# Performance work log

Measured on AMD Instinct MI355X. Metric: run time of the kernel, lower is better.

The kernel has to match this reference:

```python
import jax, jax.numpy as jnp
import numpy as np

D_MODEL = 1024
D_STATE = 16
D_CONV = 4
D_INNER = 2048  # expand * d_model
BATCH = 2
LENGTH = 2048


def silu(u):
    return u * jax.nn.sigmoid(u)


def setup_inputs() -> dict:
    key = jax.random.key(0)
    ks = jax.random.split(key, 8)
    sc = 0.02
    x = jax.random.normal(ks[0], (BATCH, LENGTH, D_MODEL), jnp.float32)
    W_in = jax.random.normal(ks[1], (2 * D_INNER, D_MODEL), jnp.float32) * sc
    conv_w = jax.random.normal(ks[2], (D_INNER, 1, D_CONV), jnp.float32) * 0.1
    conv_b = jnp.zeros((D_INNER,), jnp.float32)
    W_x = jax.random.normal(ks[3], (D_INNER + 2 * D_STATE, D_INNER), jnp.float32) * sc
    W_dt = jax.random.normal(ks[4], (D_INNER, D_INNER), jnp.float32) * sc
    b_dt = jnp.zeros((D_INNER,), jnp.float32)
    # A = arange(1, d_state+1) repeated for each inner channel (per source init)
    A_log = jnp.log(jnp.tile(jnp.arange(1, D_STATE + 1, dtype=jnp.float32), (D_INNER, 1)))
    D = jnp.ones((D_INNER,), jnp.float32)
    W_out = jax.random.normal(ks[5], (D_MODEL, D_INNER), jnp.float32) * sc
    ln_g = jnp.ones((D_MODEL,), jnp.float32)
    ln_b = jnp.zeros((D_MODEL,), jnp.float32)
    return dict(x=x, W_in=W_in, conv_w=conv_w, conv_b=conv_b, W_x=W_x, W_dt=W_dt,
                b_dt=b_dt, A_log=A_log, D=D, W_out=W_out, ln_g=ln_g, ln_b=ln_b)


def reference(x, W_in, conv_w, conv_b, W_x, W_dt, b_dt, A_log, D, W_out, ln_g, ln_b):
    b, l, _ = x.shape
    residual = x
    # in_proj, split into x-path and gate z
    xz = x @ W_in.T  # (b, l, 2*d_inner)
    xs, z = jnp.split(xz, 2, axis=-1)
    # depthwise causal conv1d (left pad d_conv-1, take first l outputs)
    xc = jnp.transpose(xs, (0, 2, 1))  # (b, d_inner, l)
    xc = jax.lax.conv_general_dilated(
        xc, conv_w, window_strides=(1,), padding=[(D_CONV - 1, 0)],
        dimension_numbers=('NCH', 'OIH', 'NCH'), feature_group_count=D_INNER)
    xc = xc + conv_b[None, :, None]
    u = silu(jnp.transpose(xc, (0, 2, 1)))  # (b, l, d_inner)
    # SSM parameter projection
    proj = u @ W_x.T  # (b, l, d_inner + 2*d_state)
    d_in, Bm, Cm = jnp.split(proj, [D_INNER, D_INNER + D_STATE], axis=-1)
    delta = jax.nn.softplus(d_in @ W_dt.T + b_dt)  # (b, l, d_inner)
    A = -jnp.exp(A_log)  # (d_inner, d_state)
    dA = jnp.exp(delta[..., None] * A)                         # (b, l, d, n)
    dBu = delta[..., None] * Bm[:, :, None, :] * u[..., None]  # (b, l, d, n)

    def step(state, inp):
        dA_t, dBu_t, c_t = inp
        state = state * dA_t + dBu_t            # (b, d, n)
        y_t = jnp.einsum('bdn,bn->bd', state, c_t)
        return state, y_t

    init = jnp.zeros((b, D_INNER, D_STATE), x.dtype)
    _, ys = jax.lax.scan(step, init, (jnp.transpose(dA, (1, 0, 2, 3)),
                                      jnp.transpose(dBu, (1, 0, 2, 3)),
                                      jnp.transpose(Cm, (1, 0, 2))))
    y = jnp.transpose(ys, (1, 0, 2)) + u * D  # (b, l, d_inner)
    y = y * silu(z)
    out = y @ W_out.T + residual
    mu = jnp.mean(out, axis=-1, keepdims=True)
    var = jnp.var(out, axis=-1, keepdims=True)
    return (out - mu) / jnp.sqrt(var + 1e-5) * ln_g + ln_b
```

## Files before the change

### kernel.cpp

```cpp
#include <hip/hip_runtime.h>

typedef unsigned short u16;
typedef unsigned int u32;
typedef __bf16 bf16x8_t __attribute__((ext_vector_type(8)));
typedef float f32x4_t __attribute__((ext_vector_type(4)));


#define NCH 64
#define CLEN 32

__device__ __forceinline__ u16 f2bf(float f) {
  u32 u = __float_as_uint(f);
  return (u16)((u + 0x7fffu + ((u >> 16) & 1u)) >> 16);
}
__device__ __forceinline__ float bf2f(u16 h) { return __uint_as_float(((u32)h) << 16); }

__device__ __forceinline__ void async_ld16(const u16* g, u16* l) {
  __builtin_amdgcn_global_load_lds((const __attribute__((address_space(1))) void*)g,
                                   (__attribute__((address_space(3))) void*)l, 16, 0, 0);
}

__global__ void k_cvt_all(const float* __restrict__ x, u16* __restrict__ x_bf,
                          const float* __restrict__ W_in, u16* __restrict__ Win_bf,
                          const float* __restrict__ W_x, u16* __restrict__ Wx_bf,
                          const float* __restrict__ W_dt, u16* __restrict__ Wdt_bf,
                          const float* __restrict__ W_out, u16* __restrict__ Wout_bf) {
  int g = blockIdx.x * 256 + threadIdx.x;
  const float* src;
  u16* dst;
  int rel;
  bool valid = true;
  if (g < 1048576) { src = x; dst = x_bf; rel = g; }
  else if (g < 2097152) { src = W_in; dst = Win_bf; rel = g - 1048576; }
  else if (g < 3211264) { src = W_x; dst = Wx_bf; rel = g - 2097152; valid = rel < 1064960; }
  else if (g < 4259840) { src = W_dt; dst = Wdt_bf; rel = g - 3211264; }
  else if (g < 4784128) { src = W_out; dst = Wout_bf; rel = g - 4259840; }
  else return;
  u32 lo = 0, hi = 0;
  if (valid) {
    float4 v = reinterpret_cast<const float4*>(src)[rel];
    lo = (u32)f2bf(v.x) | ((u32)f2bf(v.y) << 16);
    hi = (u32)f2bf(v.z) | ((u32)f2bf(v.w) << 16);
  }
  reinterpret_cast<uint2*>(dst)[rel] = make_uint2(lo, hi);
}

__global__ void k_transpose(const u16* __restrict__ in, u16* __restrict__ out) {
  __shared__ u16 tile[64][72];
  int bx = blockIdx.x;
  int by = blockIdx.y;
  int t = threadIdx.x;
#pragma unroll
  for (int i = 0; i < 2; ++i) {
    int idx = i * 256 + t;
    int r = idx >> 3;
    int c = (idx & 7) * 8;
    *reinterpret_cast<uint4*>(&tile[r][c]) =
        *reinterpret_cast<const uint4*>(in + (size_t)(by * 64 + r) * 2048 + bx * 64 + c);
  }
  __syncthreads();
#pragma unroll
  for (int i = 0; i < 2; ++i) {
    int idx = i * 256 + t;
    int r = idx >> 3;
    int c = (idx & 7) * 8;
    u16 tmp[8];
#pragma unroll
    for (int e = 0; e < 8; ++e) tmp[e] = tile[c + e][r];
    *reinterpret_cast<uint4*>(out + (size_t)(bx * 64 + r) * 2048 + by * 64 + c) =
        *reinterpret_cast<uint4*>(tmp);
  }
}

template <bool WB, bool WF>
__global__ __launch_bounds__(256, 2) void k_gemm_bt(
    const u16* __restrict__ A, int lda, const u16* __restrict__ B, int ldb,
    float* __restrict__ Cf, int ldcf, size_t fsplit,
    u16* __restrict__ Cb, int ldc, int K) {
  __shared__ __align__(16) u16 sA[128 * 64];
  __shared__ __align__(16) u16 sB[128 * 64];
  const int tid = threadIdx.x;
  const int lane = tid & 63;
  const int wave = tid >> 6;
  const size_t tm = (size_t)blockIdx.y * 128;
  const size_t tn = (size_t)blockIdx.x * 128;
  const int kbase = blockIdx.z * K;
  const int wm = (wave & 1) * 64;
  const int wn = (wave >> 1) * 64;
  const int mrow = lane & 15;
  const int quad = lane >> 4;

  f32x4_t acc[4][4];
#pragma unroll
  for (int i = 0; i < 4; ++i)
#pragma unroll
    for (int j = 0; j < 4; ++j) {
      acc[i][j][0] = 0.f; acc[i][j][1] = 0.f; acc[i][j][2] = 0.f; acc[i][j][3] = 0.f;
    }

  for (int k0 = 0; k0 < K; k0 += 64) {
#pragma unroll
    for (int j = 0; j < 4; ++j) {
      int idx = j * 256 + tid;
      int row = idx >> 3;
      int col = (idx & 7) << 3;
      async_ld16(A + (tm + row) * (size_t)lda + (kbase + k0 + col), sA + (size_t)idx * 8);
      async_ld16(B + (tn + row) * (size_t)ldb + (kbase + k0 + col), sB + (size_t)idx * 8);
    }
    __syncthreads();
#pragma unroll
    for (int kk = 0; kk < 64; kk += 32) {
      bf16x8_t af[4], bfr[4];
#pragma unroll
      for (int i = 0; i < 4; ++i)
        af[i] = *reinterpret_cast<const bf16x8_t*>(sA + (wm + i * 16 + mrow) * 64 + kk + quad * 8);
#pragma unroll
      for (int i = 0; i < 4; ++i)
        bfr[i] = *reinterpret_cast<const bf16x8_t*>(sB + (wn + i * 16 + mrow) * 64 + kk + quad * 8);
#pragma unroll
      for (int i = 0; i < 4; ++i)
#pragma unroll
        for (int j = 0; j < 4; ++j)
          acc[i][j] = __builtin_amdgcn_mfma_f32_16x16x32_bf16(af[i], bfr[j], acc[i][j], 0, 0, 0);
    }
    __syncthreads();
  }

  if (WF) Cf += (size_t)blockIdx.z * fsplit;
#pragma unroll
  for (int i = 0; i < 4; ++i)
#pragma unroll
    for (int j = 0; j < 4; ++j) {
      size_t r0 = tm + wm + i * 16 + quad * 4;
      size_t c = tn + wn + j * 16 + mrow;
#pragma unroll
      for (int r = 0; r < 4; ++r) {
        float v = acc[i][j][r];
        if (WF) Cf[(r0 + r) * (size_t)ldcf + c] = v;
        if (WB) Cb[(r0 + r) * (size_t)ldc + c] = f2bf(v);
      }
    }
}

__global__ void k_bc_reduce(const float* __restrict__ part, float* __restrict__ projBC) {
  int g = blockIdx.x * 256 + threadIdx.x;
  int r = g >> 3, c4 = (g & 7) * 4;
  size_t idx = (size_t)r * 128 + c4;
  float4 a = *reinterpret_cast<const float4*>(part + idx);
  float4 b = *reinterpret_cast<const float4*>(part + 524288 + idx);
  float4 c = *reinterpret_cast<const float4*>(part + 1048576 + idx);
  float4 d = *reinterpret_cast<const float4*>(part + 1572864 + idx);
  float4 o;
  o.x = a.x + b.x + c.x + d.x;
  o.y = a.y + b.y + c.y + d.y;
  o.z = a.z + b.z + c.z + d.z;
  o.w = a.w + b.w + c.w + d.w;
  *reinterpret_cast<float4*>(projBC + idx) = o;
}

__global__ void k_conv_silu(const u16* __restrict__ xz, const float* __restrict__ cw,
                            const float* __restrict__ cb, u16* __restrict__ u) {
  int bl = blockIdx.x;
  int l = bl & 2047;
  int d0 = threadIdx.x * 8;
  float acc[8];
  float4 cb0 = *reinterpret_cast<const float4*>(cb + d0);
  float4 cb1 = *reinterpret_cast<const float4*>(cb + d0 + 4);
  acc[0] = cb0.x; acc[1] = cb0.y; acc[2] = cb0.z; acc[3] = cb0.w;
  acc[4] = cb1.x; acc[5] = cb1.y; acc[6] = cb1.z; acc[7] = cb1.w;
  float4 w[8];
#pragma unroll
  for (int i = 0; i < 8; ++i) w[i] = *reinterpret_cast<const float4*>(cw + (d0 + i) * 4);
#pragma unroll
  for (int k = 0; k < 4; ++k) {
    int lp = l + k - 3;
    if (lp >= 0) {
      bf16x8_t xv = *reinterpret_cast<const bf16x8_t*>(xz + ((size_t)(bl + k - 3) << 12) + d0);
#pragma unroll
      for (int i = 0; i < 8; ++i)
        acc[i] += (float)xv[i] * reinterpret_cast<const float*>(&w[i])[k];
    }
  }
  u16 tmp[8];
#pragma unroll
  for (int i = 0; i < 8; ++i) {
    float s = acc[i] / (1.f + __expf(-acc[i]));
    tmp[i] = f2bf(s);
  }
  *reinterpret_cast<uint4*>(u + ((size_t)bl << 11) + d0) = *reinterpret_cast<uint4*>(tmp);
}

__device__ __forceinline__ float softplus_fast(float x) {
  return __logf(1.f + __expf(x));
}

__global__ void k_scan1(const u16* __restrict__ dpre, const float* __restrict__ bdt,
                        const u16* __restrict__ u, const float* __restrict__ projBC,
                        const float* __restrict__ A_log, float* __restrict__ sF,
                        float* __restrict__ aF) {
  int d = blockIdx.x * 256 + threadIdx.x;
  int c = blockIdx.y, b = blockIdx.z;
  float A[16], s[16], ap[16];
#pragma unroll
  for (int q = 0; q < 4; ++q) {
    float4 al = reinterpret_cast<const float4*>(A_log + d * 16)[q];
    A[q * 4 + 0] = -__expf(al.x); A[q * 4 + 1] = -__expf(al.y);
    A[q * 4 + 2] = -__expf(al.z); A[q * 4 + 3] = -__expf(al.w);
  }
#pragma unroll
  for (int n = 0; n < 16; ++n) { s[n] = 0.f; ap[n] = 1.f; }
  float bd = bdt[d];
  int t0 = c * CLEN;
  for (int t = t0; t < t0 + CLEN; ++t) {
    size_t rb = (size_t)(b * 2048 + t);
    float delta = softplus_fast(bf2f(dpre[rb * 2048 + d]) + bd);
    float du = delta * bf2f(u[rb * 2048 + d]);
    const float4* Bp = reinterpret_cast<const float4*>(projBC + rb * 128);
    float4 B0 = Bp[0], B1 = Bp[1], B2 = Bp[2], B3 = Bp[3];
    float Bv[16] = {B0.x, B0.y, B0.z, B0.w, B1.x, B1.y, B1.z, B1.w,
                    B2.x, B2.y, B2.z, B2.w, B3.x, B3.y, B3.z, B3.w};
#pragma unroll
    for (int n = 0; n < 16; ++n) {
      float dA = __expf(delta * A[n]);
      s[n] = fmaf(s[n], dA, du * Bv[n]);
      ap[n] *= dA;
    }
  }
  size_t o = ((size_t)((b * NCH + c) * 2048 + d)) << 4;
#pragma unroll
  for (int q = 0; q < 4; ++q) {
    reinterpret_cast<float4*>(sF + o)[q] = make_float4(s[q * 4], s[q * 4 + 1], s[q * 4 + 2], s[q * 4 + 3]);
    reinterpret_cast<float4*>(aF + o)[q] = make_float4(ap[q * 4], ap[q * 4 + 1], ap[q * 4 + 2], ap[q * 4 + 3]);
  }
}

__global__ void k_scan_carry(const float* __restrict__ sF, const float* __restrict__ aF,
                             float* __restrict__ carry) {
  int g = blockIdx.x * 256 + threadIdx.x;
  int b = g >> 15;
  int dn = g & 32767;
  float S = 0.f;
#pragma unroll 4
  for (int c = 0; c < NCH; ++c) {
    size_t idx = ((size_t)(b * NCH + c) << 15) + dn;
    carry[idx] = S;
    S = S * aF[idx] + sF[idx];
  }
}

__global__ void k_scan3(const u16* __restrict__ dpre, const float* __restrict__ bdt,
                        const u16* __restrict__ u, const float* __restrict__ projBC,
                        const float* __restrict__ A_log, const float* __restrict__ carry,
                        const float* __restrict__ Dvec, const u16* __restrict__ xz,
                        u16* __restrict__ ybf) {
  int d = blockIdx.x * 256 + threadIdx.x;
  int c = blockIdx.y, b = blockIdx.z;
  float A[16], s[16];
#pragma unroll
  for (int q = 0; q < 4; ++q) {
    float4 al = reinterpret_cast<const float4*>(A_log + d * 16)[q];
    A[q * 4 + 0] = -__expf(al.x); A[q * 4 + 1] = -__expf(al.y);
    A[q * 4 + 2] = -__expf(al.z); A[q * 4 + 3] = -__expf(al.w);
  }
  size_t o = ((size_t)((b * NCH + c) * 2048 + d)) << 4;
#pragma unroll
  for (int q = 0; q < 4; ++q) {
    float4 cv = reinterpret_cast<const float4*>(carry + o)[q];
    s[q * 4] = cv.x; s[q * 4 + 1] = cv.y; s[q * 4 + 2] = cv.z; s[q * 4 + 3] = cv.w;
  }
  float bd = bdt[d];
  float Dd = Dvec[d];
  int t0 = c * CLEN;
  for (int t = t0; t < t0 + CLEN; ++t) {
    size_t rb = (size_t)(b * 2048 + t);
    float delta = softplus_fast(bf2f(dpre[rb * 2048 + d]) + bd);
    float uv = bf2f(u[rb * 2048 + d]);
    float du = delta * uv;
    const float4* Bp = reinterpret_cast<const float4*>(projBC + rb * 128);
    float4 B0 = Bp[0], B1 = Bp[1], B2 = Bp[2], B3 = Bp[3];
    float4 C0 = Bp[4], C1 = Bp[5], C2 = Bp[6], C3 = Bp[7];
    float Bv[16] = {B0.x, B0.y, B0.z, B0.w, B1.x, B1.y, B1.z, B1.w,
                    B2.x, B2.y, B2.z, B2.w, B3.x, B3.y, B3.z, B3.w};
    float Cv[16] = {C0.x, C0.y, C0.z, C0.w, C1.x, C1.y, C1.z, C1.w,
                    C2.x, C2.y, C2.z, C2.w, C3.x, C3.y, C3.z, C3.w};
    float yv = 0.f;
#pragma unroll
    for (int n = 0; n < 16; ++n) {
      float dA = __expf(delta * A[n]);
      s[n] = fmaf(s[n], dA, du * Bv[n]);
      yv = fmaf(s[n], Cv[n], yv);
    }
    yv += uv * Dd;
    float z = bf2f(xz[(rb << 12) + 2048 + d]);
    yv *= z / (1.f + __expf(-z));
    ybf[rb * 2048 + d] = f2bf(yv);
  }
}

__global__ void k_ln(const float* __restrict__ pre, const float* __restrict__ x,
                     const float* __restrict__ gam, const float* __restrict__ bet,
                     float* __restrict__ out) {
  int row = blockIdx.x, tid = threadIdx.x;
  size_t base = (size_t)row * 1024 + tid * 4;
  float4 v = *reinterpret_cast<const float4*>(pre + base);
  float4 p1 = *reinterpret_cast<const float4*>(pre + 4194304 + base);
  float4 r = *reinterpret_cast<const float4*>(x + base);
  v.x += p1.x + r.x; v.y += p1.y + r.y; v.z += p1.z + r.z; v.w += p1.w + r.w;
  float s = v.x + v.y + v.z + v.w;
  float s2 = v.x * v.x + v.y * v.y + v.z * v.z + v.w * v.w;
#pragma unroll
  for (int o = 32; o >= 1; o >>= 1) {
    s += __shfl_xor(s, o);
    s2 += __shfl_xor(s2, o);
  }
  __shared__ float red[8];
  int lane = tid & 63, wv = tid >> 6;
  if (lane == 0) { red[wv] = s; red[4 + wv] = s2; }
  __syncthreads();
  s = red[0] + red[1] + red[2] + red[3];
  s2 = red[4] + red[5] + red[6] + red[7];
  float mu = s * (1.f / 1024.f);
  float var = s2 * (1.f / 1024.f) - mu * mu;
  float rstd = rsqrtf(var + 1e-5f);
  float4 gg = *reinterpret_cast<const float4*>(gam + tid * 4);
  float4 bb = *reinterpret_cast<const float4*>(bet + tid * 4);
  float4 o;
  o.x = (v.x - mu) * rstd * gg.x + bb.x;
  o.y = (v.y - mu) * rstd * gg.y + bb.y;
  o.z = (v.z - mu) * rstd * gg.z + bb.z;
  o.w = (v.w - mu) * rstd * gg.w + bb.w;
  *reinterpret_cast<float4*>(out + base) = o;
}

extern "C" void kernel_launch(void* const* d_in, const int* in_sizes, int n_in,
                              void* d_out, int out_size, void* d_ws, size_t ws_size,
                              hipStream_t stream) {
  (void)in_sizes; (void)n_in; (void)out_size; (void)ws_size;
  const float* x = (const float*)d_in[0];
  const float* W_in = (const float*)d_in[1];
  const float* conv_w = (const float*)d_in[2];
  const float* conv_b = (const float*)d_in[3];
  const float* W_x = (const float*)d_in[4];
  const float* W_dt = (const float*)d_in[5];
  const float* b_dt = (const float*)d_in[6];
  const float* A_log = (const float*)d_in[7];
  const float* Dv = (const float*)d_in[8];
  const float* W_out = (const float*)d_in[9];
  const float* ln_g = (const float*)d_in[10];
  const float* ln_b = (const float*)d_in[11];
  float* out = (float*)d_out;

  char* p = (char*)d_ws;
  u16* xz_bf = (u16*)p;      p += (size_t)4096 * 4096 * 2;
  u16* u_bf = (u16*)p;       p += (size_t)4096 * 2048 * 2;
  float* projBC = (float*)p; p += (size_t)4096 * 128 * 4;
  u16* dpre_bf = (u16*)p;    p += (size_t)4096 * 2048 * 2;
  u16* ybf = (u16*)p;        p += (size_t)4096 * 2048 * 2;
  float* sF = (float*)p;     p += (size_t)2 * NCH * 2048 * 16 * 4;
  float* aF = (float*)p;     p += (size_t)2 * NCH * 2048 * 16 * 4;
  float* carry = (float*)p;  p += (size_t)2 * NCH * 2048 * 16 * 4;
  u16* Wx_bf = (u16*)p;      p += (size_t)2176 * 2048 * 2;
  u16* WxT_bf = (u16*)p;     p += (size_t)2048 * 2048 * 2;
  u16* Weff_bf = (u16*)p;    p += (size_t)2048 * 2048 * 2;
  u16* Wdt_bf = (u16*)p;     p += (size_t)2048 * 2048 * 2;
  u16* Wout_bf = (u16*)p;    p += (size_t)1024 * 2048 * 2;
  u16* x_bf = (u16*)p;       p += (size_t)4096 * 1024 * 2;
  u16* Win_bf = (u16*)p;     p += (size_t)4096 * 1024 * 2;
  float* BCpart = sF;
  float* outpre = sF;

  k_cvt_all<<<18688, 256, 0, stream>>>(x, x_bf, W_in, Win_bf, W_x, Wx_bf, W_dt, Wdt_bf,
                                       W_out, Wout_bf);
  k_transpose<<<dim3(32, 32), 256, 0, stream>>>(Wx_bf, WxT_bf);
  k_gemm_bt<true, false><<<dim3(16, 16), 256, 0, stream>>>(
      Wdt_bf, 2048, WxT_bf, 2048, nullptr, 0, 0, Weff_bf, 2048, 2048);
  k_gemm_bt<true, false><<<dim3(32, 32), 256, 0, stream>>>(
      x_bf, 1024, Win_bf, 1024, nullptr, 0, 0, xz_bf, 4096, 1024);
  k_conv_silu<<<4096, 256, 0, stream>>>(xz_bf, conv_w, conv_b, u_bf);
  k_gemm_bt<false, true><<<dim3(1, 32, 4), 256, 0, stream>>>(
      u_bf, 2048, Wx_bf + (size_t)2048 * 2048, 2048, BCpart, 128, (size_t)4096 * 128,
      nullptr, 0, 512);
  k_bc_reduce<<<128, 256, 0, stream>>>(BCpart, projBC);
  k_gemm_bt<true, false><<<dim3(16, 32), 256, 0, stream>>>(
      u_bf, 2048, Weff_bf, 2048, nullptr, 0, 0, dpre_bf, 2048, 2048);
  k_scan1<<<dim3(8, NCH, 2), 256, 0, stream>>>(dpre_bf, b_dt, u_bf, projBC, A_log, sF, aF);
  k_scan_carry<<<256, 256, 0, stream>>>(sF, aF, carry);
  k_scan3<<<dim3(8, NCH, 2), 256, 0, stream>>>(dpre_bf, b_dt, u_bf, projBC, A_log, carry,
                                               Dv, xz_bf, ybf);
  k_gemm_bt<false, true><<<dim3(8, 32, 2), 256, 0, stream>>>(
      ybf, 2048, Wout_bf, 2048, outpre, 1024, (size_t)4096 * 1024, nullptr, 0, 1024);
  k_ln<<<4096, 256, 0, stream>>>(outpre, x, ln_g, ln_b, out);
}
```

Measured before the change: 453.3 us.

## Merge prep kernels, co-launch independent GEMMs, fold B/C projection into delta GEMM

```diff
diff --git a/kernel.cpp b/kernel.cpp
--- a/kernel.cpp
+++ b/kernel.cpp
@@ -20,71 +20,73 @@
                                    (__attribute__((address_space(3))) void*)l, 16, 0, 0);
 }
 
-__global__ void k_cvt_all(const float* __restrict__ x, u16* __restrict__ x_bf,
-                          const float* __restrict__ W_in, u16* __restrict__ Win_bf,
-                          const float* __restrict__ W_x, u16* __restrict__ Wx_bf,
-                          const float* __restrict__ W_dt, u16* __restrict__ Wdt_bf,
-                          const float* __restrict__ W_out, u16* __restrict__ Wout_bf) {
-  int g = blockIdx.x * 256 + threadIdx.x;
-  const float* src;
-  u16* dst;
-  int rel;
-  bool valid = true;
-  if (g < 1048576) { src = x; dst = x_bf; rel = g; }
-  else if (g < 2097152) { src = W_in; dst = Win_bf; rel = g - 1048576; }
-  else if (g < 3211264) { src = W_x; dst = Wx_bf; rel = g - 2097152; valid = rel < 1064960; }
-  else if (g < 4259840) { src = W_dt; dst = Wdt_bf; rel = g - 3211264; }
-  else if (g < 4784128) { src = W_out; dst = Wout_bf; rel = g - 4259840; }
-  else return;
-  u32 lo = 0, hi = 0;
-  if (valid) {
-    float4 v = reinterpret_cast<const float4*>(src)[rel];
-    lo = (u32)f2bf(v.x) | ((u32)f2bf(v.y) << 16);
-    hi = (u32)f2bf(v.z) | ((u32)f2bf(v.w) << 16);
-  }
-  reinterpret_cast<uint2*>(dst)[rel] = make_uint2(lo, hi);
-}
-
-__global__ void k_transpose(const u16* __restrict__ in, u16* __restrict__ out) {
+__global__ void k_prep(const float* __restrict__ x, u16* __restrict__ x_bf,
+                       const float* __restrict__ W_in, u16* __restrict__ Win_bf,
+                       const float* __restrict__ W_dt, u16* __restrict__ Wdt_bf,
+                       const float* __restrict__ W_out, u16* __restrict__ Wout_bf,
+                       const float* __restrict__ W_x, u16* __restrict__ WxT,
+                       u16* __restrict__ Weff_ext) {
   __shared__ u16 tile[64][72];
-  int bx = blockIdx.x;
-  int by = blockIdx.y;
-  int t = threadIdx.x;
-#pragma unroll
-  for (int i = 0; i < 2; ++i) {
-    int idx = i * 256 + t;
-    int r = idx >> 3;
-    int c = (idx & 7) * 8;
-    *reinterpret_cast<uint4*>(&tile[r][c]) =
-        *reinterpret_cast<const uint4*>(in + (size_t)(by * 64 + r) * 2048 + bx * 64 + c);
-  }
-  __syncthreads();
-#pragma unroll
-  for (int i = 0; i < 2; ++i) {
-    int idx = i * 256 + t;
-    int r = idx >> 3;
-    int c = (idx & 7) * 8;
-    u16 tmp[8];
-#pragma unroll
-    for (int e = 0; e < 8; ++e) tmp[e] = tile[c + e][r];
-    *reinterpret_cast<uint4*>(out + (size_t)(bx * 64 + r) * 2048 + by * 64 + c) =
-        *reinterpret_cast<uint4*>(tmp);
+  int blk = blockIdx.x;
+  if (blk < 14592) {
+    int g = blk * 256 + threadIdx.x;
+    const float* src;
+    u16* dst;
+    int rel;
+    bool rd = true;
+    if (g < 1048576) { src = x; dst = x_bf; rel = g; }
+    else if (g < 2097152) { src = W_in; dst = Win_bf; rel = g - 1048576; }
+    else if (g < 3145728) { src = W_dt; dst = Wdt_bf; rel = g - 2097152; }
+    else if (g < 3670016) { src = W_out; dst = Wout_bf; rel = g - 3145728; }
+    else if (g < 3686400) { src = W_x + 4194304; dst = Weff_ext + (size_t)2048 * 2048; rel = g - 3670016; }
+    else { dst = Weff_ext + (size_t)2080 * 2048; rel = g - 3686400; rd = false; src = x; }
+    u32 lo = 0, hi = 0;
+    if (rd) {
+      float4 v = reinterpret_cast<const float4*>(src)[rel];
+      lo = (u32)f2bf(v.x) | ((u32)f2bf(v.y) << 16);
+      hi = (u32)f2bf(v.z) | ((u32)f2bf(v.w) << 16);
+    }
+    reinterpret_cast<uint2*>(dst)[rel] = make_uint2(lo, hi);
+  } else {
+    int bid = blk - 14592;
+    int bx = bid & 31;
+    int by = bid >> 5;
+    int t = threadIdx.x;
+#pragma unroll
+    for (int i = 0; i < 4; ++i) {
+      int idx = i * 256 + t;
+      int r = idx >> 4;
+      int c = (idx & 15) * 4;
+      float4 v = *reinterpret_cast<const float4*>(W_x + (size_t)(by * 64 + r) * 2048 + bx * 64 + c);
+      tile[r][c] = f2bf(v.x); tile[r][c + 1] = f2bf(v.y);
+      tile[r][c + 2] = f2bf(v.z); tile[r][c + 3] = f2bf(v.w);
+    }
+    __syncthreads();
+#pragma unroll
+    for (int i = 0; i < 2; ++i) {
+      int idx = i * 256 + t;
+      int r = idx >> 3;
+      int c = (idx & 7) * 8;
+      u16 tmp[8];
+#pragma unroll
+      for (int e = 0; e < 8; ++e) tmp[e] = tile[c + e][r];
+      *reinterpret_cast<uint4*>(WxT + (size_t)(bx * 64 + r) * 2048 + by * 64 + c) =
+          *reinterpret_cast<uint4*>(tmp);
+    }
   }
 }
 
 template <bool WB, bool WF>
-__global__ __launch_bounds__(256, 2) void k_gemm_bt(
+__device__ __forceinline__ void gemm_tile(
+    u16* sA, u16* sB, int bx, int by, int kbase,
     const u16* __restrict__ A, int lda, const u16* __restrict__ B, int ldb,
-    float* __restrict__ Cf, int ldcf, size_t fsplit,
+    float* __restrict__ Cf, int fcol0, int ldcf,
     u16* __restrict__ Cb, int ldc, int K) {
-  __shared__ __align__(16) u16 sA[128 * 64];
-  __shared__ __align__(16) u16 sB[128 * 64];
   const int tid = threadIdx.x;
   const int lane = tid & 63;
   const int wave = tid >> 6;
-  const size_t tm = (size_t)blockIdx.y * 128;
-  const size_t tn = (size_t)blockIdx.x * 128;
-  const int kbase = blockIdx.z * K;
+  const size_t tm = (size_t)by * 128;
+  const size_t tn = (size_t)bx * 128;
   const int wm = (wave & 1) * 64;
   const int wn = (wave >> 1) * 64;
   const int mrow = lane & 15;
@@ -126,7 +128,6 @@
     __syncthreads();
   }
 
-  if (WF) Cf += (size_t)blockIdx.z * fsplit;
 #pragma unroll
   for (int i = 0; i < 4; ++i)
 #pragma unroll
@@ -136,26 +137,37 @@
 #pragma unroll
       for (int r = 0; r < 4; ++r) {
         float v = acc[i][j][r];
-        if (WF) Cf[(r0 + r) * (size_t)ldcf + c] = v;
-        if (WB) Cb[(r0 + r) * (size_t)ldc + c] = f2bf(v);
+        if (WF && (int)c >= fcol0) Cf[(r0 + r) * (size_t)ldcf + (c - fcol0)] = v;
+        if (WB && (int)c < fcol0) Cb[(r0 + r) * (size_t)ldc + c] = f2bf(v);
       }
     }
 }
 
-__global__ void k_bc_reduce(const float* __restrict__ part, float* __restrict__ projBC) {
-  int g = blockIdx.x * 256 + threadIdx.x;
-  int r = g >> 3, c4 = (g & 7) * 4;
-  size_t idx = (size_t)r * 128 + c4;
-  float4 a = *reinterpret_cast<const float4*>(part + idx);
-  float4 b = *reinterpret_cast<const float4*>(part + 524288 + idx);
-  float4 c = *reinterpret_cast<const float4*>(part + 1048576 + idx);
-  float4 d = *reinterpret_cast<const float4*>(part + 1572864 + idx);
-  float4 o;
-  o.x = a.x + b.x + c.x + d.x;
-  o.y = a.y + b.y + c.y + d.y;
-  o.z = a.z + b.z + c.z + d.z;
-  o.w = a.w + b.w + c.w + d.w;
-  *reinterpret_cast<float4*>(projBC + idx) = o;
+template <bool WB, bool WF>
+__global__ __launch_bounds__(256, 2) void k_gemm(
+    const u16* __restrict__ A, int lda, const u16* __restrict__ B, int ldb,
+    float* __restrict__ Cf, int fcol0, int ldcf, size_t fsplit,
+    u16* __restrict__ Cb, int ldc, int K) {
+  __shared__ __align__(16) u16 sA[128 * 64];
+  __shared__ __align__(16) u16 sB[128 * 64];
+  gemm_tile<WB, WF>(sA, sB, blockIdx.x, blockIdx.y, blockIdx.z * K, A, lda, B, ldb,
+                    Cf + (size_t)blockIdx.z * fsplit, fcol0, ldcf, Cb, ldc, K);
+}
+
+__global__ __launch_bounds__(256, 2) void k_gemm_dual(
+    const u16* __restrict__ A1, const u16* __restrict__ B1, u16* __restrict__ C1,
+    const u16* __restrict__ A2, const u16* __restrict__ B2, u16* __restrict__ C2) {
+  __shared__ __align__(16) u16 sA[128 * 64];
+  __shared__ __align__(16) u16 sB[128 * 64];
+  int b = blockIdx.x;
+  if (b < 1024) {
+    gemm_tile<true, false>(sA, sB, b & 31, b >> 5, 0, A1, 1024, B1, 1024,
+                           nullptr, 1 << 30, 0, C1, 4096, 1024);
+  } else {
+    int b2 = b - 1024;
+    gemm_tile<true, false>(sA, sB, b2 & 15, b2 >> 4, 0, A2, 2048, B2, 2048,
+                           nullptr, 1 << 30, 0, C2, 2048, 2048);
+  }
 }
 
 __global__ void k_conv_silu(const u16* __restrict__ xz, const float* __restrict__ cw,
@@ -359,35 +371,25 @@
   float* sF = (float*)p;     p += (size_t)2 * NCH * 2048 * 16 * 4;
   float* aF = (float*)p;     p += (size_t)2 * NCH * 2048 * 16 * 4;
   float* carry = (float*)p;  p += (size_t)2 * NCH * 2048 * 16 * 4;
-  u16* Wx_bf = (u16*)p;      p += (size_t)2176 * 2048 * 2;
   u16* WxT_bf = (u16*)p;     p += (size_t)2048 * 2048 * 2;
-  u16* Weff_bf = (u16*)p;    p += (size_t)2048 * 2048 * 2;
+  u16* Weff_ext = (u16*)p;   p += (size_t)2176 * 2048 * 2;
   u16* Wdt_bf = (u16*)p;     p += (size_t)2048 * 2048 * 2;
   u16* Wout_bf = (u16*)p;    p += (size_t)1024 * 2048 * 2;
   u16* x_bf = (u16*)p;       p += (size_t)4096 * 1024 * 2;
   u16* Win_bf = (u16*)p;     p += (size_t)4096 * 1024 * 2;
-  float* BCpart = sF;
   float* outpre = sF;
 
-  k_cvt_all<<<18688, 256, 0, stream>>>(x, x_bf, W_in, Win_bf, W_x, Wx_bf, W_dt, Wdt_bf,
-                                       W_out, Wout_bf);
-  k_transpose<<<dim3(32, 32), 256, 0, stream>>>(Wx_bf, WxT_bf);
-  k_gemm_bt<true, false><<<dim3(16, 16), 256, 0, stream>>>(
-      Wdt_bf, 2048, WxT_bf, 2048, nullptr, 0, 0, Weff_bf, 2048, 2048);
-  k_gemm_bt<true, false><<<dim3(32, 32), 256, 0, stream>>>(
-      x_bf, 1024, Win_bf, 1024, nullptr, 0, 0, xz_bf, 4096, 1024);
+  k_prep<<<15616, 256, 0, stream>>>(x, x_bf, W_in, Win_bf, W_dt, Wdt_bf, W_out, Wout_bf,
+                                    W_x, WxT_bf, Weff_ext);
+  k_gemm_dual<<<1280, 256, 0, stream>>>(x_bf, Win_bf, xz_bf, Wdt_bf, WxT_bf, Weff_ext);
   k_conv_silu<<<4096, 256, 0, stream>>>(xz_bf, conv_w, conv_b, u_bf);
-  k_gemm_bt<false, true><<<dim3(1, 32, 4), 256, 0, stream>>>(
-      u_bf, 2048, Wx_bf + (size_t)2048 * 2048, 2048, BCpart, 128, (size_t)4096 * 128,
-      nullptr, 0, 512);
-  k_bc_reduce<<<128, 256, 0, stream>>>(BCpart, projBC);
-  k_gemm_bt<true, false><<<dim3(16, 32), 256, 0, stream>>>(
-      u_bf, 2048, Weff_bf, 2048, nullptr, 0, 0, dpre_bf, 2048, 2048);
+  k_gemm<true, true><<<dim3(17, 32), 256, 0, stream>>>(
+      u_bf, 2048, Weff_ext, 2048, projBC, 2048, 128, 0, dpre_bf, 2048, 2048);
   k_scan1<<<dim3(8, NCH, 2), 256, 0, stream>>>(dpre_bf, b_dt, u_bf, projBC, A_log, sF, aF);
   k_scan_carry<<<256, 256, 0, stream>>>(sF, aF, carry);
   k_scan3<<<dim3(8, NCH, 2), 256, 0, stream>>>(dpre_bf, b_dt, u_bf, projBC, A_log, carry,
                                                Dv, xz_bf, ybf);
-  k_gemm_bt<false, true><<<dim3(8, 32, 2), 256, 0, stream>>>(
-      ybf, 2048, Wout_bf, 2048, outpre, 1024, (size_t)4096 * 1024, nullptr, 0, 1024);
+  k_gemm<false, true><<<dim3(8, 32, 2), 256, 0, stream>>>(
+      ybf, 2048, Wout_bf, 2048, outpre, 0, 1024, (size_t)4096 * 1024, nullptr, 0, 1024);
   k_ln<<<4096, 256, 0, stream>>>(outpre, x, ln_g, ln_b, out);
 }
```

Measured after the change: 433.2 us. -4.4%, faster.
